# Performance work log

Measured on AMD Instinct MI355X. Metric: run time of the kernel, lower is better.

The kernel has to match this reference:

```python
import jax, jax.numpy as jnp
import numpy as np

B, T, D, H = 8, 1024, 512, 8
CH = D // H          # chunk_size = d_model // num_heads
PAD = 0              # pad_token_id
MAX_TRANS = 1024     # translen cap from source
NINF = float('-inf')


def setup_inputs() -> dict:
    key = jax.random.key(0)
    ks = jax.random.split(key, 8)
    features = jax.random.normal(ks[0], (B, T, D), jnp.float32)
    pos_embed = jax.random.normal(ks[1], (B, T, D), jnp.float32)
    tokens = jax.random.randint(ks[2], (B, T), 0, 32000, dtype=jnp.int32)
    Wq = jax.random.normal(ks[3], (D, 2 * D), jnp.float32) * 0.02
    bq = jnp.zeros((D,), jnp.float32)
    Wk = jax.random.normal(ks[4], (D, 2 * D), jnp.float32) * 0.02
    bk = jnp.zeros((D,), jnp.float32)
    Wg = jax.random.normal(ks[5], (H, 2 * D), jnp.float32) * 0.02
    bg = jnp.zeros((H,), jnp.float32)
    return dict(features=features, pos_embed=pos_embed, tokens=tokens,
                Wq=Wq, bq=bq, Wk=Wk, bk=bk, Wg=Wg, bg=bg)


def _safe_log_softmax(x, axis):
    # matches torch F.log_softmax followed by re-masking: rows that are all -inf stay -inf
    m = jnp.max(x, axis=axis, keepdims=True)
    allinf = jnp.isneginf(m)
    m_safe = jnp.where(allinf, 0.0, m)
    lse = m_safe + jnp.log(jnp.sum(jnp.exp(x - m_safe), axis=axis, keepdims=True))
    lse = jnp.where(allinf, 0.0, lse)
    return x - lse


def _safe_logsumexp(x, axis):
    # matches the custom logsumexp helper in the source (all -inf -> -inf, no nan)
    m = jnp.max(x, axis=axis)
    mask = jnp.isneginf(m)
    m_safe = jnp.where(mask, 0.0, m)
    s = jnp.sum(jnp.exp(x - jnp.expand_dims(m_safe, axis)), axis=axis)
    return jnp.log(jnp.where(mask, 1.0, s)) + jnp.where(mask, NINF, m_safe)


def reference(features, pos_embed, tokens, Wq, bq, Wk, bk, Wg, bg):
    # features_withpos = cat(decoder_out, link positional embedding)  -> [B, T, 2D]
    f = jnp.concatenate([features, pos_embed], axis=-1)
    q = (f @ Wq.T + bq).reshape(B, T, H, CH)
    k = (f @ Wk.T + bk).reshape(B, T, H, CH)
    log_gates = jax.nn.log_softmax(f @ Wg.T + bg, axis=-1)  # [B, T, H]
    # einsum 'bicf,bjcf->bijc' with c = head chunk
    scores = jnp.einsum('bihc,bjhc->bijh', q, k) / np.float32(np.sqrt(CH))  # [B,T,T,H]

    translen = min(MAX_TRANS, T - 1)
    n_valid = jnp.sum(tokens != PAD, axis=-1)  # [B]
    # banded indices: position i links to positions i+1 .. i+translen
    band_idx = jnp.arange(T)[:, None] + jnp.arange(translen)[None, :] + 1  # [T, translen]
    invalid = band_idx[None, :, :] >= n_valid[:, None, None]               # [B, T, translen]
    idx_c = jnp.where(invalid, 0, band_idx[None, :, :])
    idx_full = jnp.broadcast_to(idx_c[..., None], (B, T, translen, H))
    extract = jnp.take_along_axis(scores, idx_full, axis=2)                # [B,T,translen,H]
    extract = jnp.where(invalid[..., None], NINF, extract)
    # normalize over transition axis, then mask fully-invalid rows back to -inf
    extract = _safe_log_softmax(extract, axis=2)
    nouse = jnp.all(invalid, axis=-1)                                      # [B, T]
    extract = jnp.where(nouse[:, :, None, None], NINF, extract)
    # head-gated logsumexp over heads -> banded links [B, T, translen]
    links_band = _safe_logsumexp(extract + log_gates[:, :, None, :], axis=-1)
    # restore_valid_links: scatter band back to full [B, T, T] (-inf elsewhere)
    rel = jnp.arange(T)[None, :] - jnp.arange(T)[:, None] - 1              # [T, T]
    valid = (rel >= 0) & (rel < translen)
    rel_c = jnp.clip(rel, 0, translen - 1)
    rel_full = jnp.broadcast_to(rel_c[None, :, :], (B, T, T))
    out = jnp.take_along_axis(links_band, rel_full, axis=2)
    return jnp.where(valid[None, :, :], out, NINF)
```

## Files before the change

### kernel.cpp

```cpp
#include <hip/hip_runtime.h>
#include <math.h>

#define BATCH 8
#define T 1024
#define NH 8
#define NROW 8192
#define NEG_INF (-INFINITY)
#define SENT (-1.0e30f)
#define SC 0.180336880f
#define LOG2E 1.442695041f

typedef __attribute__((ext_vector_type(8))) short short8;
typedef __attribute__((ext_vector_type(4))) float f32x4;

__device__ __forceinline__ ushort f2bf(float x) {
  uint u = __float_as_uint(x);
  return (ushort)((u + 0x7FFFu + ((u >> 16) & 1u)) >> 16);
}
__device__ __forceinline__ uint pack2(float a, float b) {
  return (uint)f2bf(a) | ((uint)f2bf(b) << 16);
}
__device__ __forceinline__ void gl_lds16(const ushort* g, ushort* l) {
  __builtin_amdgcn_global_load_lds(
      (const __attribute__((address_space(1))) unsigned int*)g,
      (__attribute__((address_space(3))) unsigned int*)l, 16, 0, 0);
}

__global__ __launch_bounds__(256) void k_nvalid(const int* __restrict__ tokens,
                                                int* __restrict__ nv) {
  int b = blockIdx.x, t = threadIdx.x;
  int cnt = 0;
  for (int i = t; i < T; i += 256) cnt += (tokens[b * T + i] != 0) ? 1 : 0;
  __shared__ int s[256];
  s[t] = cnt;
  __syncthreads();
  for (int st = 128; st > 0; st >>= 1) {
    if (t < st) s[t] += s[t + st];
    __syncthreads();
  }
  if (t == 0) nv[b] = s[0];
}

__global__ __launch_bounds__(256) void k_prep_w(const float* __restrict__ Wq,
                                                const float* __restrict__ Wk,
                                                ushort* __restrict__ Wbf) {
  const int gid = blockIdx.x * 256 + threadIdx.x;
  const int e0 = gid * 8;
  const int n = e0 >> 10, k = e0 & 1023;
  const float* src = (n < 512) ? (Wq + (size_t)n * 1024 + k)
                               : (Wk + (size_t)(n - 512) * 1024 + k);
  float4 a = *(const float4*)src;
  float4 b = *(const float4*)(src + 4);
  uint4 o;
  o.x = pack2(a.x, a.y); o.y = pack2(a.z, a.w);
  o.z = pack2(b.x, b.y); o.w = pack2(b.z, b.w);
  *(uint4*)(Wbf + (size_t)n * 1024 + k) = o;
}

__global__ __launch_bounds__(256) void k_prep_fg(
    const float* __restrict__ feat, const float* __restrict__ pos,
    const float* __restrict__ Wg, const float* __restrict__ bg,
    ushort* __restrict__ fbf, float* __restrict__ gout) {
  __shared__ __align__(16) float Ws[8192];
  const int tid = threadIdx.x;
#pragma unroll
  for (int u = 0; u < 8; ++u)
    ((float4*)Ws)[u * 256 + tid] = ((const float4*)Wg)[u * 256 + tid];
  __syncthreads();

  const int w = tid >> 6, l = tid & 63;
  const int c0 = l * 16;
  const int row0 = blockIdx.x * 8 + w * 2;

  float4 f[2][4];
#pragma unroll
  for (int r = 0; r < 2; ++r) {
    const int row = row0 + r;
    const float* src = (c0 < 512) ? (feat + (size_t)row * 512 + c0)
                                  : (pos + (size_t)row * 512 + (c0 - 512));
#pragma unroll
    for (int q4 = 0; q4 < 4; ++q4) f[r][q4] = *(const float4*)(src + q4 * 4);
    uint4 o0, o1;
    o0.x = pack2(f[r][0].x, f[r][0].y); o0.y = pack2(f[r][0].z, f[r][0].w);
    o0.z = pack2(f[r][1].x, f[r][1].y); o0.w = pack2(f[r][1].z, f[r][1].w);
    o1.x = pack2(f[r][2].x, f[r][2].y); o1.y = pack2(f[r][2].z, f[r][2].w);
    o1.z = pack2(f[r][3].x, f[r][3].y); o1.w = pack2(f[r][3].z, f[r][3].w);
    *(uint4*)(fbf + (size_t)row * 1024 + c0) = o0;
    *(uint4*)(fbf + (size_t)row * 1024 + c0 + 8) = o1;
  }

  float s[2][8];
#pragma unroll
  for (int h = 0; h < 8; ++h) {
    const float* wg = Ws + h * 1024 + c0;
    float4 w0 = *(const float4*)(wg + 0);
    float4 w1 = *(const float4*)(wg + 4);
    float4 w2 = *(const float4*)(wg + 8);
    float4 w3 = *(const float4*)(wg + 12);
#pragma unroll
    for (int r = 0; r < 2; ++r)
      s[r][h] = f[r][0].x * w0.x + f[r][0].y * w0.y + f[r][0].z * w0.z + f[r][0].w * w0.w
              + f[r][1].x * w1.x + f[r][1].y * w1.y + f[r][1].z * w1.z + f[r][1].w * w1.w
              + f[r][2].x * w2.x + f[r][2].y * w2.y + f[r][2].z * w2.z + f[r][2].w * w2.w
              + f[r][3].x * w3.x + f[r][3].y * w3.y + f[r][3].z * w3.z + f[r][3].w * w3.w;
  }
#pragma unroll
  for (int m = 1; m < 64; m <<= 1)
#pragma unroll
    for (int r = 0; r < 2; ++r)
#pragma unroll
      for (int h = 0; h < 8; ++h) s[r][h] += __shfl_xor(s[r][h], m, 64);
  if (l == 0) {
#pragma unroll
    for (int r = 0; r < 2; ++r) {
      float lg[8], mx = -1e30f;
#pragma unroll
      for (int h = 0; h < 8; ++h) { lg[h] = s[r][h] + bg[h]; mx = fmaxf(mx, lg[h]); }
      float sum = 0.f;
#pragma unroll
      for (int h = 0; h < 8; ++h) sum += __expf(lg[h] - mx);
      const float lse = mx + __logf(sum);
#pragma unroll
      for (int h = 0; h < 8; ++h) gout[(size_t)(row0 + r) * 8 + h] = lg[h] - lse;
    }
  }
}

__global__ __launch_bounds__(256) void k_gemm(
    const ushort* __restrict__ fbf, const ushort* __restrict__ Wbf,
    const float* __restrict__ bq, const float* __restrict__ bk,
    ushort* __restrict__ qbuf, ushort* __restrict__ kbuf) {
  const int g = blockIdx.x + 8 * blockIdx.y;
  const int wid = (g & 7) * 64 + (g >> 3);
  const int n0 = (wid & 7) * 128;
  const int m0 = (wid >> 3) * 128;
  const int tid = threadIdx.x;
  const int w = tid >> 6, l = tid & 63;
  const int lo = l & 15, quad = l >> 4;
  const int wm0 = (w >> 1) * 64, wn0 = (w & 1) * 64;

  __shared__ ushort As[128 * 64];
  __shared__ ushort Bs[128 * 64];

  f32x4 acc[4][4];
#pragma unroll
  for (int i = 0; i < 4; ++i)
#pragma unroll
    for (int j = 0; j < 4; ++j) acc[i][j] = (f32x4){0.f, 0.f, 0.f, 0.f};

  const int c8 = (tid & 7) * 8;
  const int r0 = tid >> 3;
  ushort* lA = As + (size_t)w * 512;
  ushort* lB = Bs + (size_t)w * 512;

  for (int k0 = 0; k0 < 1024; k0 += 64) {
    __syncthreads();
#pragma unroll
    for (int u = 0; u < 4; ++u) {
      gl_lds16(fbf + (size_t)(m0 + u * 32 + r0) * 1024 + k0 + c8, lA + u * 2048);
      gl_lds16(Wbf + (size_t)(n0 + u * 32 + r0) * 1024 + k0 + c8, lB + u * 2048);
    }
    __syncthreads();
#pragma unroll
    for (int kk = 0; kk < 2; ++kk) {
      short8 af[4], bfr[4];
#pragma unroll
      for (int mi = 0; mi < 4; ++mi)
        af[mi] = *(const short8*)(As + (size_t)(wm0 + mi * 16 + lo) * 64 + kk * 32 + quad * 8);
#pragma unroll
      for (int ni = 0; ni < 4; ++ni)
        bfr[ni] = *(const short8*)(Bs + (size_t)(wn0 + ni * 16 + lo) * 64 + kk * 32 + quad * 8);
#pragma unroll
      for (int mi = 0; mi < 4; ++mi)
#pragma unroll
        for (int ni = 0; ni < 4; ++ni)
          acc[mi][ni] = __builtin_amdgcn_mfma_f32_16x16x32_bf16(bfr[ni], af[mi], acc[mi][ni], 0, 0, 0);
    }
  }

  float4 bias4[4];
#pragma unroll
  for (int ni = 0; ni < 4; ++ni) {
    const int gn = n0 + wn0 + ni * 16 + quad * 4;
    bias4[ni] = *(const float4*)((gn < 512) ? (bq + gn) : (bk + gn - 512));
  }
#pragma unroll
  for (int mi = 0; mi < 4; ++mi) {
    const int m = m0 + wm0 + mi * 16 + lo;
#pragma unroll
    for (int ni = 0; ni < 4; ++ni) {
      const int gn = n0 + wn0 + ni * 16 + quad * 4;
      ushort* dst = (gn < 512) ? (qbuf + (size_t)m * 512 + gn)
                               : (kbuf + (size_t)m * 512 + gn - 512);
      ushort4 o;
      o.x = f2bf(acc[mi][ni][0] + bias4[ni].x);
      o.y = f2bf(acc[mi][ni][1] + bias4[ni].y);
      o.z = f2bf(acc[mi][ni][2] + bias4[ni].z);
      o.w = f2bf(acc[mi][ni][3] + bias4[ni].w);
      *(ushort4*)dst = o;
    }
  }
}

__global__ __launch_bounds__(256) void k_pass1(
    const ushort* __restrict__ q, const ushort* __restrict__ kv,
    const float* __restrict__ g, const int* __restrict__ nvp,
    float* __restrict__ Wt) {
  const int it = blockIdx.x, h = blockIdx.y, b = blockIdx.z;
  const int nv = nvp[b];
  const int i0 = it * 64;
  const int tid = threadIdx.x;
  const int w = tid >> 6, l = tid & 63;
  const int lo = l & 15, quad = l >> 4;

  __shared__ ushort Ks[2][64 * 64];

  const int i = i0 + w * 16 + lo;
  const ushort* qp = q + (size_t)(b * T + i) * 512 + h * 64 + quad * 8;
  const short8 a0 = *(const short8*)qp;
  const short8 a1 = *(const short8*)(qp + 32);

  float lsum = 0.f;
  const int ntile = ((nv + 63) >> 6) - it;

  if (ntile > 0) {
    auto stage = [&](int buf, int jt) {
#pragma unroll
      for (int u = 0; u < 2; ++u) {
        const int s = u * 256 + tid;
        const int row = s >> 3, c = s & 7;
        gl_lds16(kv + (size_t)(b * T + jt * 64 + row) * 512 + h * 64 + ((c ^ (row & 7)) * 8),
                 Ks[buf] + (size_t)(u * 256 + w * 64) * 8);
      }
    };
    stage(0, it);
    __syncthreads();
    for (int s = 0; s < ntile; ++s) {
      if (s + 1 < ntile) stage((s + 1) & 1, it + s + 1);
      const ushort* kbase = Ks[s & 1];
      const int j0 = (it + s) * 64;
      const bool diag = (s == 0);
      const bool masked = diag | (j0 + 64 > nv);
#pragma unroll
      for (int ni = 0; ni < 4; ++ni) {
        if (diag && ni < w) continue;
        const int rw = ni * 16 + lo;
        const short8 b0 = *(const short8*)(kbase + (size_t)rw * 64 + ((quad ^ (rw & 7)) * 8));
        const short8 b1 = *(const short8*)(kbase + (size_t)rw * 64 + (((4 + quad) ^ (rw & 7)) * 8));
        f32x4 acc = (f32x4){0.f, 0.f, 0.f, 0.f};
        acc = __builtin_amdgcn_mfma_f32_16x16x32_bf16(b0, a0, acc, 0, 0, 0);
        acc = __builtin_amdgcn_mfma_f32_16x16x32_bf16(b1, a1, acc, 0, 0, 0);
        if (!masked) {
#pragma unroll
          for (int r = 0; r < 4; ++r) lsum += __builtin_amdgcn_exp2f(acc[r] * SC);
        } else {
          const int jb = j0 + ni * 16 + quad * 4;
#pragma unroll
          for (int r = 0; r < 4; ++r) {
            const int j = jb + r;
            if (j > i && j < nv) lsum += __builtin_amdgcn_exp2f(acc[r] * SC);
          }
        }
      }
      __syncthreads();
    }
  }

  lsum += __shfl_xor(lsum, 16, 64);
  lsum += __shfl_xor(lsum, 32, 64);
  if (quad == 0) {
    const size_t row = (size_t)(b * T) + i;
    Wt[(size_t)h * NROW + row] =
        (lsum > 0.f) ? (g[row * 8 + h] - __logf(lsum)) : NEG_INF;
  }
}

__global__ __launch_bounds__(256) void k_pass2(
    const ushort* __restrict__ q, const ushort* __restrict__ kv,
    const float* __restrict__ Wt, const int* __restrict__ nvp,
    float* __restrict__ out) {
  const int jt = blockIdx.x, it = blockIdx.y, b = blockIdx.z;
  const int nv = nvp[b];
  const int i0 = it * 64, j0 = jt * 64;
  const int tid = threadIdx.x;

  if (jt < it || j0 >= nv) {
    const int r0 = tid >> 4, c0 = (tid & 15) * 4;
    float4 v; v.x = v.y = v.z = v.w = SENT;
#pragma unroll
    for (int u = 0; u < 4; ++u)
      *(float4*)(out + ((size_t)(b * T + i0 + r0 + u * 16)) * T + j0 + c0) = v;
    return;
  }

  const int w = tid >> 6, l = tid & 63;
  const int lo = l & 15, quad = l >> 4;
  const int i = i0 + w * 16 + lo;

  __shared__ ushort Ks[64 * 512];

#pragma unroll
  for (int u = 0; u < 16; ++u) {
    const int row = u * 4 + w;
    gl_lds16(kv + (size_t)(b * T + j0 + row) * 512 + ((l ^ (row & 7)) * 8),
             Ks + (size_t)(u * 256 + w * 64) * 8);
  }

  const ushort* qb = q + (size_t)(b * T + i) * 512 + quad * 8;
  short8 qa0[8], qa1[8];
  float wl[8];
#pragma unroll
  for (int h = 0; h < 8; ++h) {
    qa0[h] = *(const short8*)(qb + h * 64);
    qa1[h] = *(const short8*)(qb + h * 64 + 32);
    wl[h] = Wt[(size_t)h * NROW + b * T + i] * LOG2E;
  }

  float se[4][4];
#pragma unroll
  for (int a = 0; a < 4; ++a)
#pragma unroll
    for (int c = 0; c < 4; ++c) se[a][c] = 0.f;

  __syncthreads();

#pragma unroll
  for (int h = 0; h < 8; ++h) {
#pragma unroll
    for (int ni = 0; ni < 4; ++ni) {
      const int rw = ni * 16 + lo;
      const int cs0 = (h * 8 + quad) ^ (rw & 7);
      const int cs1 = (h * 8 + 4 + quad) ^ (rw & 7);
      const short8 b0 = *(const short8*)(Ks + (size_t)rw * 512 + cs0 * 8);
      const short8 b1 = *(const short8*)(Ks + (size_t)rw * 512 + cs1 * 8);
      f32x4 acc = (f32x4){0.f, 0.f, 0.f, 0.f};
      acc = __builtin_amdgcn_mfma_f32_16x16x32_bf16(b0, qa0[h], acc, 0, 0, 0);
      acc = __builtin_amdgcn_mfma_f32_16x16x32_bf16(b1, qa1[h], acc, 0, 0, 0);
#pragma unroll
      for (int r = 0; r < 4; ++r)
        se[ni][r] += __builtin_amdgcn_exp2f(acc[r] * SC + wl[h]);
    }
  }

  const size_t orow = ((size_t)(b * T + i)) * T;
#pragma unroll
  for (int ni = 0; ni < 4; ++ni) {
    const int jb = j0 + ni * 16 + quad * 4;
    float4 v;
    v.x = (jb + 0 > i && jb + 0 < nv) ? fmaxf(__logf(se[ni][0]), SENT) : SENT;
    v.y = (jb + 1 > i && jb + 1 < nv) ? fmaxf(__logf(se[ni][1]), SENT) : SENT;
    v.z = (jb + 2 > i && jb + 2 < nv) ? fmaxf(__logf(se[ni][2]), SENT) : SENT;
    v.w = (jb + 3 > i && jb + 3 < nv) ? fmaxf(__logf(se[ni][3]), SENT) : SENT;
    *(float4*)(out + orow + jb) = v;
  }
}

extern "C" void kernel_launch(void* const* d_in, const int* in_sizes, int n_in,
                              void* d_out, int out_size, void* d_ws, size_t ws_size,
                              hipStream_t stream) {
  (void)in_sizes; (void)n_in; (void)out_size; (void)ws_size;
  const float* feat = (const float*)d_in[0];
  const float* pos  = (const float*)d_in[1];
  const int* tokens = (const int*)d_in[2];
  const float* Wq = (const float*)d_in[3];
  const float* bq = (const float*)d_in[4];
  const float* Wk = (const float*)d_in[5];
  const float* bk = (const float*)d_in[6];
  const float* Wg = (const float*)d_in[7];
  const float* bg = (const float*)d_in[8];
  float* out = (float*)d_out;

  ushort* qbuf = (ushort*)d_ws;
  ushort* kbuf = qbuf + (size_t)NROW * 512;
  ushort* Wbf  = kbuf + (size_t)NROW * 512;
  float*  gbuf = (float*)(Wbf + (size_t)1024 * 1024);
  float*  Wt   = gbuf + (size_t)NROW * NH;
  int*    nv   = (int*)(Wt + (size_t)NH * NROW);

  ushort* fbf = (ushort*)d_out;

  k_nvalid<<<dim3(BATCH), dim3(256), 0, stream>>>(tokens, nv);
  k_prep_w<<<dim3(512), dim3(256), 0, stream>>>(Wq, Wk, Wbf);
  k_prep_fg<<<dim3(1024), dim3(256), 0, stream>>>(feat, pos, Wg, bg, fbf, gbuf);
  k_gemm<<<dim3(8, 64), dim3(256), 0, stream>>>(fbf, Wbf, bq, bk, qbuf, kbuf);
  k_pass1<<<dim3(16, NH, BATCH), dim3(256), 0, stream>>>(qbuf, kbuf, gbuf, nv, Wt);
  k_pass2<<<dim3(16, 16, BATCH), dim3(256), 0, stream>>>(qbuf, kbuf, Wt, nv, out);
}
```

Baseline: 189.8 us.

## Double-buffer LDS staging in GEMM and pass2, merge prep kernels into one launch

The three prep kernels (token count, weight conversion, feature/gate prep) are merged into one launch that dispatches on block index, saving two launches. The GEMM gets double-buffered LDS tiles so the next K-slice loads while MFMAs run on the current one. Pass2 stops loading the full 64x512 K tile up front and streams one head's 64x64 slice at a time through two small LDS buffers. This cuts shared memory from 64KB to 16KB, which should raise occupancy and overlap loads with compute, at the cost of a barrier per head.

Result: faster. 182.5 us (-3.9%).

```diff
diff --git a/kernel.cpp b/kernel.cpp
--- a/kernel.cpp
+++ b/kernel.cpp
@@ -26,103 +26,103 @@
       (__attribute__((address_space(3))) unsigned int*)l, 16, 0, 0);
 }
 
-__global__ __launch_bounds__(256) void k_nvalid(const int* __restrict__ tokens,
-                                                int* __restrict__ nv) {
-  int b = blockIdx.x, t = threadIdx.x;
-  int cnt = 0;
-  for (int i = t; i < T; i += 256) cnt += (tokens[b * T + i] != 0) ? 1 : 0;
-  __shared__ int s[256];
-  s[t] = cnt;
-  __syncthreads();
-  for (int st = 128; st > 0; st >>= 1) {
-    if (t < st) s[t] += s[t + st];
+__global__ __launch_bounds__(256) void k_prep(
+    const float* __restrict__ feat, const float* __restrict__ pos,
+    const int* __restrict__ tokens,
+    const float* __restrict__ Wq, const float* __restrict__ Wk,
+    const float* __restrict__ Wg, const float* __restrict__ bg,
+    ushort* __restrict__ fbf, ushort* __restrict__ Wbf,
+    float* __restrict__ gout, int* __restrict__ nvout) {
+  const int bid = blockIdx.x;
+  const int tid = threadIdx.x;
+
+  if (bid < 1024) {
+    __shared__ __align__(16) float Ws[8192];
+#pragma unroll
+    for (int u = 0; u < 8; ++u)
+      ((float4*)Ws)[u * 256 + tid] = ((const float4*)Wg)[u * 256 + tid];
     __syncthreads();
-  }
-  if (t == 0) nv[b] = s[0];
-}
-
-__global__ __launch_bounds__(256) void k_prep_w(const float* __restrict__ Wq,
-                                                const float* __restrict__ Wk,
-                                                ushort* __restrict__ Wbf) {
-  const int gid = blockIdx.x * 256 + threadIdx.x;
-  const int e0 = gid * 8;
-  const int n = e0 >> 10, k = e0 & 1023;
-  const float* src = (n < 512) ? (Wq + (size_t)n * 1024 + k)
-                               : (Wk + (size_t)(n - 512) * 1024 + k);
-  float4 a = *(const float4*)src;
-  float4 b = *(const float4*)(src + 4);
-  uint4 o;
-  o.x = pack2(a.x, a.y); o.y = pack2(a.z, a.w);
-  o.z = pack2(b.x, b.y); o.w = pack2(b.z, b.w);
-  *(uint4*)(Wbf + (size_t)n * 1024 + k) = o;
-}
-
-__global__ __launch_bounds__(256) void k_prep_fg(
-    const float* __restrict__ feat, const float* __restrict__ pos,
-    const float* __restrict__ Wg, const float* __restrict__ bg,
-    ushort* __restrict__ fbf, float* __restrict__ gout) {
-  __shared__ __align__(16) float Ws[8192];
-  const int tid = threadIdx.x;
-#pragma unroll
-  for (int u = 0; u < 8; ++u)
-    ((float4*)Ws)[u * 256 + tid] = ((const float4*)Wg)[u * 256 + tid];
-  __syncthreads();
-
-  const int w = tid >> 6, l = tid & 63;
-  const int c0 = l * 16;
-  const int row0 = blockIdx.x * 8 + w * 2;
-
-  float4 f[2][4];
-#pragma unroll
-  for (int r = 0; r < 2; ++r) {
-    const int row = row0 + r;
-    const float* src = (c0 < 512) ? (feat + (size_t)row * 512 + c0)
-                                  : (pos + (size_t)row * 512 + (c0 - 512));
-#pragma unroll
-    for (int q4 = 0; q4 < 4; ++q4) f[r][q4] = *(const float4*)(src + q4 * 4);
-    uint4 o0, o1;
-    o0.x = pack2(f[r][0].x, f[r][0].y); o0.y = pack2(f[r][0].z, f[r][0].w);
-    o0.z = pack2(f[r][1].x, f[r][1].y); o0.w = pack2(f[r][1].z, f[r][1].w);
-    o1.x = pack2(f[r][2].x, f[r][2].y); o1.y = pack2(f[r][2].z, f[r][2].w);
-    o1.z = pack2(f[r][3].x, f[r][3].y); o1.w = pack2(f[r][3].z, f[r][3].w);
-    *(uint4*)(fbf + (size_t)row * 1024 + c0) = o0;
-    *(uint4*)(fbf + (size_t)row * 1024 + c0 + 8) = o1;
-  }
-
-  float s[2][8];
-#pragma unroll
-  for (int h = 0; h < 8; ++h) {
-    const float* wg = Ws + h * 1024 + c0;
-    float4 w0 = *(const float4*)(wg + 0);
-    float4 w1 = *(const float4*)(wg + 4);
-    float4 w2 = *(const float4*)(wg + 8);
-    float4 w3 = *(const float4*)(wg + 12);
-#pragma unroll
-    for (int r = 0; r < 2; ++r)
-      s[r][h] = f[r][0].x * w0.x + f[r][0].y * w0.y + f[r][0].z * w0.z + f[r][0].w * w0.w
-              + f[r][1].x * w1.x + f[r][1].y * w1.y + f[r][1].z * w1.z + f[r][1].w * w1.w
-              + f[r][2].x * w2.x + f[r][2].y * w2.y + f[r][2].z * w2.z + f[r][2].w * w2.w
-              + f[r][3].x * w3.x + f[r][3].y * w3.y + f[r][3].z * w3.z + f[r][3].w * w3.w;
-  }
-#pragma unroll
-  for (int m = 1; m < 64; m <<= 1)
-#pragma unroll
-    for (int r = 0; r < 2; ++r)
-#pragma unroll
-      for (int h = 0; h < 8; ++h) s[r][h] += __shfl_xor(s[r][h], m, 64);
-  if (l == 0) {
+
+    const int w = tid >> 6, l = tid & 63;
+    const int c0 = l * 16;
+    const int row0 = bid * 8 + w * 2;
+
+    float4 f[2][4];
 #pragma unroll
     for (int r = 0; r < 2; ++r) {
-      float lg[8], mx = -1e30f;
-#pragma unroll
-      for (int h = 0; h < 8; ++h) { lg[h] = s[r][h] + bg[h]; mx = fmaxf(mx, lg[h]); }
-      float sum = 0.f;
-#pragma unroll
-      for (int h = 0; h < 8; ++h) sum += __expf(lg[h] - mx);
-      const float lse = mx + __logf(sum);
-#pragma unroll
-      for (int h = 0; h < 8; ++h) gout[(size_t)(row0 + r) * 8 + h] = lg[h] - lse;
-    }
+      const int row = row0 + r;
+      const float* src = (c0 < 512) ? (feat + (size_t)row * 512 + c0)
+                                    : (pos + (size_t)row * 512 + (c0 - 512));
+#pragma unroll
+      for (int q4 = 0; q4 < 4; ++q4) f[r][q4] = *(const float4*)(src + q4 * 4);
+      uint4 o0, o1;
+      o0.x = pack2(f[r][0].x, f[r][0].y); o0.y = pack2(f[r][0].z, f[r][0].w);
+      o0.z = pack2(f[r][1].x, f[r][1].y); o0.w = pack2(f[r][1].z, f[r][1].w);
+      o1.x = pack2(f[r][2].x, f[r][2].y); o1.y = pack2(f[r][2].z, f[r][2].w);
+      o1.z = pack2(f[r][3].x, f[r][3].y); o1.w = pack2(f[r][3].z, f[r][3].w);
+      *(uint4*)(fbf + (size_t)row * 1024 + c0) = o0;
+      *(uint4*)(fbf + (size_t)row * 1024 + c0 + 8) = o1;
+    }
+
+    float s[2][8];
+#pragma unroll
+    for (int h = 0; h < 8; ++h) {
+      const float* wg = Ws + h * 1024 + c0;
+      float4 w0 = *(const float4*)(wg + 0);
+      float4 w1 = *(const float4*)(wg + 4);
+      float4 w2 = *(const float4*)(wg + 8);
+      float4 w3 = *(const float4*)(wg + 12);
+#pragma unroll
+      for (int r = 0; r < 2; ++r)
+        s[r][h] = f[r][0].x * w0.x + f[r][0].y * w0.y + f[r][0].z * w0.z + f[r][0].w * w0.w
+                + f[r][1].x * w1.x + f[r][1].y * w1.y + f[r][1].z * w1.z + f[r][1].w * w1.w
+                + f[r][2].x * w2.x + f[r][2].y * w2.y + f[r][2].z * w2.z + f[r][2].w * w2.w
+                + f[r][3].x * w3.x + f[r][3].y * w3.y + f[r][3].z * w3.z + f[r][3].w * w3.w;
+    }
+#pragma unroll
+    for (int m = 1; m < 64; m <<= 1)
+#pragma unroll
+      for (int r = 0; r < 2; ++r)
+#pragma unroll
+        for (int h = 0; h < 8; ++h) s[r][h] += __shfl_xor(s[r][h], m, 64);
+    if (l == 0) {
+#pragma unroll
+      for (int r = 0; r < 2; ++r) {
+        float lg[8], mx = -1e30f;
+#pragma unroll
+        for (int h = 0; h < 8; ++h) { lg[h] = s[r][h] + bg[h]; mx = fmaxf(mx, lg[h]); }
+        float sum = 0.f;
+#pragma unroll
+        for (int h = 0; h < 8; ++h) sum += __expf(lg[h] - mx);
+        const float lse = mx + __logf(sum);
+#pragma unroll
+        for (int h = 0; h < 8; ++h) gout[(size_t)(row0 + r) * 8 + h] = lg[h] - lse;
+      }
+    }
+  } else if (bid < 1536) {
+    const int gid = (bid - 1024) * 256 + tid;
+    const int e0 = gid * 8;
+    const int n = e0 >> 10, k = e0 & 1023;
+    const float* src = (n < 512) ? (Wq + (size_t)n * 1024 + k)
+                                 : (Wk + (size_t)(n - 512) * 1024 + k);
+    float4 a = *(const float4*)src;
+    float4 b = *(const float4*)(src + 4);
+    uint4 o;
+    o.x = pack2(a.x, a.y); o.y = pack2(a.z, a.w);
+    o.z = pack2(b.x, b.y); o.w = pack2(b.z, b.w);
+    *(uint4*)(Wbf + (size_t)n * 1024 + k) = o;
+  } else {
+    const int b = bid - 1536;
+    int cnt = 0;
+    for (int i = tid; i < T; i += 256) cnt += (tokens[b * T + i] != 0) ? 1 : 0;
+    __shared__ int s[256];
+    s[tid] = cnt;
+    __syncthreads();
+    for (int st = 128; st > 0; st >>= 1) {
+      if (tid < st) s[tid] += s[tid + st];
+      __syncthreads();
+    }
+    if (tid == 0) nvout[b] = s[0];
   }
 }
 
@@ -139,8 +139,8 @@
   const int lo = l & 15, quad = l >> 4;
   const int wm0 = (w >> 1) * 64, wn0 = (w & 1) * 64;
 
-  __shared__ ushort As[128 * 64];
-  __shared__ ushort Bs[128 * 64];
+  __shared__ ushort As[2][128 * 64];
+  __shared__ ushort Bs[2][128 * 64];
 
   f32x4 acc[4][4];
 #pragma unroll
@@ -150,32 +150,40 @@
 
   const int c8 = (tid & 7) * 8;
   const int r0 = tid >> 3;
-  ushort* lA = As + (size_t)w * 512;
-  ushort* lB = Bs + (size_t)w * 512;
-
+
+  auto stage = [&](int buf, int k0) {
+#pragma unroll
+    for (int u = 0; u < 4; ++u) {
+      gl_lds16(fbf + (size_t)(m0 + u * 32 + r0) * 1024 + k0 + c8,
+               As[buf] + (size_t)w * 512 + u * 2048);
+      gl_lds16(Wbf + (size_t)(n0 + u * 32 + r0) * 1024 + k0 + c8,
+               Bs[buf] + (size_t)w * 512 + u * 2048);
+    }
+  };
+
+  stage(0, 0);
+  int cur = 0;
   for (int k0 = 0; k0 < 1024; k0 += 64) {
     __syncthreads();
-#pragma unroll
-    for (int u = 0; u < 4; ++u) {
-      gl_lds16(fbf + (size_t)(m0 + u * 32 + r0) * 1024 + k0 + c8, lA + u * 2048);
-      gl_lds16(Wbf + (size_t)(n0 + u * 32 + r0) * 1024 + k0 + c8, lB + u * 2048);
-    }
-    __syncthreads();
+    if (k0 + 64 < 1024) stage(cur ^ 1, k0 + 64);
+    const ushort* pA = As[cur];
+    const ushort* pB = Bs[cur];
 #pragma unroll
     for (int kk = 0; kk < 2; ++kk) {
       short8 af[4], bfr[4];
 #pragma unroll
       for (int mi = 0; mi < 4; ++mi)
-        af[mi] = *(const short8*)(As + (size_t)(wm0 + mi * 16 + lo) * 64 + kk * 32 + quad * 8);
+        af[mi] = *(const short8*)(pA + (size_t)(wm0 + mi * 16 + lo) * 64 + kk * 32 + quad * 8);
 #pragma unroll
       for (int ni = 0; ni < 4; ++ni)
-        bfr[ni] = *(const short8*)(Bs + (size_t)(wn0 + ni * 16 + lo) * 64 + kk * 32 + quad * 8);
+        bfr[ni] = *(const short8*)(pB + (size_t)(wn0 + ni * 16 + lo) * 64 + kk * 32 + quad * 8);
 #pragma unroll
       for (int mi = 0; mi < 4; ++mi)
 #pragma unroll
         for (int ni = 0; ni < 4; ++ni)
           acc[mi][ni] = __builtin_amdgcn_mfma_f32_16x16x32_bf16(bfr[ni], af[mi], acc[mi][ni], 0, 0, 0);
     }
+    cur ^= 1;
   }
 
   float4 bias4[4];
@@ -297,14 +305,19 @@
   const int lo = l & 15, quad = l >> 4;
   const int i = i0 + w * 16 + lo;
 
-  __shared__ ushort Ks[64 * 512];
-
-#pragma unroll
-  for (int u = 0; u < 16; ++u) {
-    const int row = u * 4 + w;
-    gl_lds16(kv + (size_t)(b * T + j0 + row) * 512 + ((l ^ (row & 7)) * 8),
-             Ks + (size_t)(u * 256 + w * 64) * 8);
-  }
+  __shared__ ushort Ks[2][64 * 64];
+
+  auto stage = [&](int buf, int h) {
+#pragma unroll
+    for (int u = 0; u < 2; ++u) {
+      const int s = u * 256 + tid;
+      const int row = s >> 3, c = s & 7;
+      gl_lds16(kv + (size_t)(b * T + j0 + row) * 512 + h * 64 + ((c ^ (row & 7)) * 8),
+               Ks[buf] + (size_t)(u * 256 + w * 64) * 8);
+    }
+  };
+
+  stage(0, 0);
 
   const ushort* qb = q + (size_t)(b * T + i) * 512 + quad * 8;
   short8 qa0[8], qa1[8];
@@ -326,13 +339,13 @@
 
 #pragma unroll
   for (int h = 0; h < 8; ++h) {
+    if (h < 7) stage((h + 1) & 1, h + 1);
+    const ushort* kbase = Ks[h & 1];
 #pragma unroll
     for (int ni = 0; ni < 4; ++ni) {
       const int rw = ni * 16 + lo;
-      const int cs0 = (h * 8 + quad) ^ (rw & 7);
-      const int cs1 = (h * 8 + 4 + quad) ^ (rw & 7);
-      const short8 b0 = *(const short8*)(Ks + (size_t)rw * 512 + cs0 * 8);
-      const short8 b1 = *(const short8*)(Ks + (size_t)rw * 512 + cs1 * 8);
+      const short8 b0 = *(const short8*)(kbase + (size_t)rw * 64 + ((quad ^ (rw & 7)) * 8));
+      const short8 b1 = *(const short8*)(kbase + (size_t)rw * 64 + (((4 + quad) ^ (rw & 7)) * 8));
       f32x4 acc = (f32x4){0.f, 0.f, 0.f, 0.f};
       acc = __builtin_amdgcn_mfma_f32_16x16x32_bf16(b0, qa0[h], acc, 0, 0, 0);
       acc = __builtin_amdgcn_mfma_f32_16x16x32_bf16(b1, qa1[h], acc, 0, 0, 0);
@@ -340,6 +353,7 @@
       for (int r = 0; r < 4; ++r)
         se[ni][r] += __builtin_amdgcn_exp2f(acc[r] * SC + wl[h]);
     }
+    if (h < 7) __syncthreads();
   }
 
   const size_t orow = ((size_t)(b * T + i)) * T;
@@ -379,9 +393,8 @@
 
   ushort* fbf = (ushort*)d_out;
 
-  k_nvalid<<<dim3(BATCH), dim3(256), 0, stream>>>(tokens, nv);
-  k_prep_w<<<dim3(512), dim3(256), 0, stream>>>(Wq, Wk, Wbf);
-  k_prep_fg<<<dim3(1024), dim3(256), 0, stream>>>(feat, pos, Wg, bg, fbf, gbuf);
+  k_prep<<<dim3(1544), dim3(256), 0, stream>>>(feat, pos, tokens, Wq, Wk, Wg, bg,
+                                               fbf, Wbf, gbuf, nv);
   k_gemm<<<dim3(8, 64), dim3(256), 0, stream>>>(fbf, Wbf, bq, bk, qbuf, kbuf);
   k_pass1<<<dim3(16, NH, BATCH), dim3(256), 0, stream>>>(qbuf, kbuf, gbuf, nv, Wt);
   k_pass2<<<dim3(16, 16, BATCH), dim3(256), 0, stream>>>(qbuf, kbuf, Wt, nv, out);
```
